# Optimization experiments

Measured on AMD Instinct MI355X. Metric: run time of the kernel, lower is better.

## Reference

```python
import jax, jax.numpy as jnp
import numpy as np

MODES1 = 16
MODES2 = 16
KX_SIGMA = 1.0
B, T, H, W, C = 4, 32, 128, 128, 1

KY_KERNEL = np.array([[0.01, 0.02, 0.04, 0.02, 0.01],
                      [0.02, 0.06, 0.09, 0.06, 0.02],
                      [0.04, 0.09, 0.16, 0.09, 0.04],
                      [0.02, 0.06, 0.09, 0.06, 0.02],
                      [0.01, 0.02, 0.04, 0.02, 0.01]], dtype=np.float32)


def _spectral_mix(x, w1, w2):
    # x: (B,T,H,W,C); w1,w2: complex (C,C,m1,m2). FFT-mode-truncated mixing.
    b, t, h, w, c = x.shape
    xc = jnp.transpose(x, (0, 1, 4, 2, 3))            # (B,T,C,H,W)
    x_ft = jnp.fft.rfft2(xc)                          # (B,T,C,H,W//2+1)
    wr = w // 2 + 1
    out_ft = jnp.zeros((b, t, c, h, wr), dtype=x_ft.dtype)
    top = jnp.einsum('btixy,ioxy->btoxy', x_ft[:, :, :, :MODES1, :MODES2], w1)
    bot = jnp.einsum('btixy,ioxy->btoxy', x_ft[:, :, :, h - MODES1:, :MODES2], w2)
    out_ft = out_ft.at[:, :, :, :MODES1, :MODES2].set(top)
    out_ft = out_ft.at[:, :, :, h - MODES1:, :MODES2].set(bot)
    out = jnp.fft.irfft2(out_ft, s=(h, w))            # (B,T,C,H,W)
    return jnp.transpose(out, (0, 1, 3, 4, 2))


def _restricted_spectral(x, scalar):
    # diagonal (identity * scalar) spectral weights == scale truncated modes
    b, t, h, w, c = x.shape
    xc = jnp.transpose(x, (0, 1, 4, 2, 3))
    x_ft = jnp.fft.rfft2(xc)
    wr = w // 2 + 1
    out_ft = jnp.zeros((b, t, c, h, wr), dtype=x_ft.dtype)
    out_ft = out_ft.at[:, :, :, :MODES1, :MODES2].set(x_ft[:, :, :, :MODES1, :MODES2] * scalar)
    out_ft = out_ft.at[:, :, :, h - MODES1:, :MODES2].set(x_ft[:, :, :, h - MODES1:, :MODES2] * scalar)
    out = jnp.fft.irfft2(out_ft, s=(h, w))
    return jnp.transpose(out, (0, 1, 3, 4, 2))


def _circular_conv(value, kernel):
    # value: (B,T,H,W,1), kernel: (kh,kw); circular-pad cross-correlation
    b, t, h, w, _ = value.shape
    kh, kw = kernel.shape
    x = value.reshape(b * t, 1, h, w)
    xp = jnp.pad(x, ((0, 0), (0, 0), (kh // 2, kh - kh // 2 - 1), (kw // 2, kw - kw // 2 - 1)), mode='wrap')
    out = jax.lax.conv_general_dilated(xp, kernel[None, None], (1, 1), 'VALID',
                                       dimension_numbers=('NCHW', 'OIHW', 'NCHW'))
    return out.reshape(b, t, h, w, 1)


def setup_inputs() -> dict:
    key = jax.random.key(0)
    ks = jax.random.split(key, 10)
    z = jax.random.normal(ks[0], (B, T, 2 * H, W, C), dtype=jnp.float32)
    scale = 1.0 / (C * C)  # torch: scale * torch.rand(cfloat) -> uniform real & imag
    u = lambda k: scale * jax.random.uniform(k, (C, C, MODES1, MODES2), dtype=jnp.float32)
    return {
        'z': z,
        'qw1r': u(ks[1]), 'qw1i': u(ks[2]), 'qw2r': u(ks[3]), 'qw2i': u(ks[4]),
        'kw1r': u(ks[5]), 'kw1i': u(ks[6]), 'kw2r': u(ks[7]), 'kw2i': u(ks[8]),
        'icl_scalar': jnp.float32(0.1),
        'ky_kernel': jnp.asarray(KY_KERNEL),
    }


def reference(z, qw1r, qw1i, qw2r, qw2i, kw1r, kw1i, kw2r, kw2i, icl_scalar, ky_kernel):
    b, t, full_h, w, c = z.shape
    h = full_h // 2
    x, y = z[:, :, :h], z[:, :, h:]
    query = _spectral_mix(x, qw1r + 1j * qw1i, qw2r + 1j * qw2i)
    keyt = _spectral_mix(x, kw1r + 1j * kw1i, kw2r + 1j * kw2i)
    value = _restricted_spectral(y, icl_scalar)
    # laplacian kernel attention scores
    q_ = query.reshape(b, t, -1)
    k_ = keyt.reshape(b, t, -1)
    diff = q_[:, :, None, :] - k_[:, None, :, :]        # (B,T,T,H*W*C)
    l2 = jnp.sqrt(jnp.sum(diff * diff, axis=-1) + 1e-8)
    kx = jnp.exp(-l2 / KX_SIGMA)                         # (B,T,T)
    # mask: M @ kx zeros out last query row
    mask = jnp.concatenate([jnp.ones((t - 1,), jnp.float32), jnp.zeros((1,), jnp.float32)])
    kx = kx * mask[None, :, None]
    vc = _circular_conv(value, ky_kernel)                # (B,T,H,W,1)
    attn_y = jnp.einsum('bthwc,btq->bqhwc', vc, kx)      # (B,T,H,W,1)
    output = jnp.concatenate([jnp.zeros_like(x), attn_y], axis=2)
    return output, kx
```

## Files before the change

### kernel.cpp

```cpp
#include <hip/hip_runtime.h>
#include <math.h>

#define FVC_OFF   0
#define PHIQ_OFF  131072
#define PHIK_OFF  262144
#define OUT_KX_OFF 4194304

#define TWOPI_128 0.049087385212340517f
#define OUT_SCALE 6.103515625e-05f

__global__ __launch_bounds__(256) void dft_rows_kernel(
    const float* __restrict__ z, float* __restrict__ Gout)
{
    __shared__ float2 tw[128];
    __shared__ float rows[16 * 132];
    __shared__ float2 tile[16 * 17];

    const int tid = threadIdx.x;
    const int img = blockIdx.x >> 3;
    const int c0  = blockIdx.x & 7;
    const int bt  = img & 127;
    const int isY = img >> 7;

    if (tid < 128) {
        float s, c;
        sincosf((float)tid * TWOPI_128, &s, &c);
        tw[tid] = make_float2(c, s);
    }
    const float* xim = z + (size_t)bt * 32768 + (size_t)isY * 16384 + (size_t)c0 * 2048;
    {
        int q0 = tid, q1 = tid + 256;
        float4 a = *(const float4*)(xim + (q0 >> 5) * 128 + (q0 & 31) * 4);
        float4 b = *(const float4*)(xim + (q1 >> 5) * 128 + (q1 & 31) * 4);
        *(float4*)(rows + (q0 >> 5) * 132 + (q0 & 31) * 4) = a;
        *(float4*)(rows + (q1 >> 5) * 132 + (q1 & 31) * 4) = b;
    }
    __syncthreads();

    const int v  = tid & 15;
    const int hl = tid >> 4;
    const float2 stp = tw[(4 * v) & 127];
    float cc = 1.f, ss = 0.f;
    float sr0 = 0.f, si0 = 0.f, sr1 = 0.f, si1 = 0.f;
    float sr2 = 0.f, si2 = 0.f, sr3 = 0.f, si3 = 0.f;
    const float4* rp = (const float4*)(rows + hl * 132);
    #pragma unroll 8
    for (int m = 0; m < 32; ++m) {
        float4 x4 = rp[m];
        sr0 = fmaf(x4.x, cc, sr0); si0 = fmaf(x4.x, ss, si0);
        sr1 = fmaf(x4.y, cc, sr1); si1 = fmaf(x4.y, ss, si1);
        sr2 = fmaf(x4.z, cc, sr2); si2 = fmaf(x4.z, ss, si2);
        sr3 = fmaf(x4.w, cc, sr3); si3 = fmaf(x4.w, ss, si3);
        float t0 = fmaf(cc, stp.x, -(ss * stp.y));
        float t1 = fmaf(cc, stp.y,  (ss * stp.x));
        cc = t0; ss = t1;
    }
    float2 w1 = tw[v];
    float2 w2 = tw[(2 * v) & 127];
    float2 w3 = tw[(3 * v) & 127];
    float gr = sr0 + sr1 * w1.x - si1 * w1.y + sr2 * w2.x - si2 * w2.y + sr3 * w3.x - si3 * w3.y;
    float gi = -(si0 + sr1 * w1.y + si1 * w1.x + sr2 * w2.y + si2 * w2.x + sr3 * w3.y + si3 * w3.x);

    tile[v * 17 + hl] = make_float2(gr, gi);
    __syncthreads();
    const int vw = tid >> 4, hw = tid & 15;
    float2 val = tile[vw * 17 + hw];
    *(float2*)(Gout + (size_t)img * 4096 + vw * 256 + (c0 * 16 + hw) * 2) = val;
}

__global__ __launch_bounds__(128) void modes_kernel(
    const float* __restrict__ Gglob,
    const float* __restrict__ qw1r, const float* __restrict__ qw1i,
    const float* __restrict__ qw2r, const float* __restrict__ qw2i,
    const float* __restrict__ kw1r, const float* __restrict__ kw1i,
    const float* __restrict__ kw2r, const float* __restrict__ kw2i,
    const float* __restrict__ icl,  const float* __restrict__ ker,
    float* __restrict__ ws)
{
    __shared__ float2 tw[128];
    __shared__ float Gbuf[4 * 260];
    __shared__ float f0r[64], f0i[64];

    const int tid = threadIdx.x;
    const int img = blockIdx.x >> 2;
    const int vg  = blockIdx.x & 3;
    const int bt  = img & 127;
    const int isY = img >> 7;

    {
        float s, c;
        sincosf((float)tid * TWOPI_128, &s, &c);
        tw[tid] = make_float2(c, s);
    }
    const float4* gsrc = (const float4*)(Gglob + (size_t)img * 4096 + (size_t)vg * 1024);
    {
        float4 a = gsrc[tid];
        float4 b = gsrc[tid + 128];
        *(float4*)(Gbuf + (tid >> 6) * 260 + (tid & 63) * 4) = a;
        *(float4*)(Gbuf + ((tid >> 6) + 2) * 260 + (tid & 63) * 4) = b;
    }
    __syncthreads();

    const int uu = tid & 31;
    const int vl = tid >> 5;
    const int v  = vg * 4 + vl;
    const int u  = (uu < 16) ? uu : uu + 96;

    const float2 stp = tw[(4 * u) & 127];
    float cc = 1.f, ss = 0.f;
    float sr[4] = {0.f, 0.f, 0.f, 0.f}, si[4] = {0.f, 0.f, 0.f, 0.f};
    const float4* gp = (const float4*)(Gbuf + vl * 260);
    #pragma unroll 8
    for (int m = 0; m < 32; ++m) {
        float4 ga = gp[2 * m];
        float4 gb = gp[2 * m + 1];
        sr[0] = fmaf(ga.x, cc, fmaf(ga.y,  ss, sr[0]));
        si[0] = fmaf(ga.y, cc, fmaf(-ga.x, ss, si[0]));
        sr[1] = fmaf(ga.z, cc, fmaf(ga.w,  ss, sr[1]));
        si[1] = fmaf(ga.w, cc, fmaf(-ga.z, ss, si[1]));
        sr[2] = fmaf(gb.x, cc, fmaf(gb.y,  ss, sr[2]));
        si[2] = fmaf(gb.y, cc, fmaf(-gb.x, ss, si[2]));
        sr[3] = fmaf(gb.z, cc, fmaf(gb.w,  ss, sr[3]));
        si[3] = fmaf(gb.w, cc, fmaf(-gb.z, ss, si[3]));
        float t0 = fmaf(cc, stp.x, -(ss * stp.y));
        float t1 = fmaf(cc, stp.y,  (ss * stp.x));
        cc = t0; ss = t1;
    }
    float mr = sr[0], mi_ = si[0];
    #pragma unroll
    for (int j = 1; j < 4; ++j) {
        float2 wj = tw[(u * j) & 127];
        mr  += sr[j] * wj.x + si[j] * wj.y;
        mi_ += si[j] * wj.x - sr[j] * wj.y;
    }

    const int wi = (uu & 15) * 16 + v;

    if (!isY) {
        float a, bi_;
        if (uu < 16) { a = qw1r[wi]; bi_ = qw1i[wi]; }
        else         { a = qw2r[wi]; bi_ = qw2i[wi]; }
        float fqr = mr * a - mi_ * bi_;
        float fqi = mr * bi_ + mi_ * a;
        if (uu < 16) { a = kw1r[wi]; bi_ = kw1i[wi]; }
        else         { a = kw2r[wi]; bi_ = kw2i[wi]; }
        float fkr = mr * a - mi_ * bi_;
        float fki = mr * bi_ + mi_ * a;

        float* PQ = ws + PHIQ_OFF + (size_t)bt * 1024;
        float* PK = ws + PHIK_OFF + (size_t)bt * 1024;
        const float c2 = 0.011048543456039806f;
        if (v >= 1) {
            int o = ((v - 1) * 32 + uu) * 2;
            PQ[o] = c2 * fqr; PQ[o + 1] = c2 * fqi;
            PK[o] = c2 * fkr; PK[o + 1] = c2 * fki;
        } else {
            f0r[uu]      = fqr; f0i[uu]      = fqi;
            f0r[32 + uu] = fkr; f0i[32 + uu] = fki;
        }
        __syncthreads();
        if (vg == 0) {
            const float c1n = 0.0078125f;
            if (tid == 0) {
                PQ[960] = c1n * f0r[0];
                PK[960] = c1n * f0r[32];
            } else if (tid <= 15) {
                int uf = tid;
                float hr = 0.5f * (f0r[uf] + f0r[32 - uf]);
                float hi = 0.5f * (f0i[uf] - f0i[32 - uf]);
                int o = 961 + (uf - 1) * 2;
                PQ[o] = c2 * hr; PQ[o + 1] = c2 * hi;
                hr = 0.5f * (f0r[32 + uf] + f0r[32 + (32 - uf)]);
                hi = 0.5f * (f0i[32 + uf] - f0i[32 + (32 - uf)]);
                PK[o] = c2 * hr; PK[o + 1] = c2 * hi;
            } else if (tid == 16) {
                PQ[991] = c2 * 0.5f * f0r[16]; PQ[992] = -c2 * 0.5f * f0i[16];
                PK[991] = c2 * 0.5f * f0r[48]; PK[992] = -c2 * 0.5f * f0i[48];
            } else if (tid < 48) {
                PQ[993 + (tid - 17)] = 0.f;
                PK[993 + (tid - 17)] = 0.f;
            }
        }
    } else {
        float s = icl[0];
        float khr = 0.f, khi = 0.f;
        #pragma unroll
        for (int a2 = 0; a2 < 5; ++a2) {
            #pragma unroll
            for (int c3 = 0; c3 < 5; ++c3) {
                float kv = ker[a2 * 5 + c3];
                float2 e = tw[(u * (a2 - 2) + v * (c3 - 2)) & 127];
                khr = fmaf(kv, e.x, khr);
                khi = fmaf(kv, e.y, khi);
            }
        }
        const int slot = uu * 16 + v;
        float* FV = ws + FVC_OFF + (size_t)bt * 1024;
        FV[slot * 2]     = s * (mr * khr - mi_ * khi);
        FV[slot * 2 + 1] = s * (mr * khi + mi_ * khr);
    }
}

__global__ __launch_bounds__(256) void dist_mix_inv_kernel(
    const float* __restrict__ ws, float* __restrict__ out)
{
    __shared__ float2 tw[128];
    __shared__ float kxs[32];
    __shared__ float fmP[32 * 36];
    __shared__ float Az[32 * 36];

    const int tid     = threadIdx.x;
    const int b       = blockIdx.x >> 7;
    const int rest    = blockIdx.x & 127;
    const int q       = rest >> 2;
    const int quarter = rest & 3;
    const size_t obase = (size_t)(b * 32 + q) * 32768;

    if (tid < 128) {
        float s, c;
        sincosf((float)tid * TWOPI_128, &s, &c);
        tw[tid] = make_float2(c, s);
    }

    {
        const float4 z4 = make_float4(0.f, 0.f, 0.f, 0.f);
        #pragma unroll
        for (int k = 0; k < 4; ++k) {
            int idx = k * 256 + tid;
            *(float4*)(out + obase + (size_t)quarter * 4096 + (size_t)idx * 4) = z4;
        }
    }

    {
        const int t = tid >> 3, seg = tid & 7;
        const float4* qp = (const float4*)(ws + PHIQ_OFF + (size_t)(b * 32 + t) * 1024) + seg * 32;
        const float4* kp = (const float4*)(ws + PHIK_OFF + (size_t)(b * 32 + q) * 1024) + seg * 32;
        float acc = 0.f;
        #pragma unroll 8
        for (int d = 0; d < 32; ++d) {
            float4 qv = qp[d], kv = kp[d];
            float d0 = qv.x - kv.x, d1 = qv.y - kv.y;
            float d2 = qv.z - kv.z, d3 = qv.w - kv.w;
            acc = fmaf(d0, d0, acc); acc = fmaf(d1, d1, acc);
            acc = fmaf(d2, d2, acc); acc = fmaf(d3, d3, acc);
        }
        acc += __shfl_xor(acc, 1);
        acc += __shfl_xor(acc, 2);
        acc += __shfl_xor(acc, 4);
        if (seg == 0) {
            float l2  = sqrtf(acc + 1e-8f);
            float kxv = (t == 31) ? 0.f : expf(-l2);
            kxs[t] = kxv;
            if (quarter == 0)
                out[OUT_KX_OFF + (b * 32 + t) * 32 + q] = kxv;
        }
    }
    __syncthreads();

    {
        float4 acc = make_float4(0.f, 0.f, 0.f, 0.f);
        const float4* FV = (const float4*)(ws + FVC_OFF) + (size_t)b * 32 * 256;
        for (int i = 0; i < 31; ++i) {
            float kv = kxs[i];
            float4 f = FV[(size_t)i * 256 + tid];
            acc.x = fmaf(kv, f.x, acc.x);
            acc.y = fmaf(kv, f.y, acc.y);
            acc.z = fmaf(kv, f.z, acc.z);
            acc.w = fmaf(kv, f.w, acc.w);
        }
        int s0 = tid * 2;
        *(float4*)(fmP + (s0 >> 4) * 36 + (s0 & 15) * 2) = acc;
    }
    __syncthreads();

    {
        const int hl = tid >> 3;
        const int v0 = (tid & 7) * 2;
        const int h  = quarter * 32 + hl;
        const float2 stp = tw[h];
        float cA = 1.f, sA = 0.f;
        const float2 ib = tw[(112 * h) & 127];
        float cB = ib.x, sB = ib.y;
        float ar0 = 0.f, ai0 = 0.f, ar1 = 0.f, ai1 = 0.f;
        #pragma unroll 4
        for (int j = 0; j < 16; ++j) {
            float4 fa = *(const float4*)(fmP + j * 36 + v0 * 2);
            ar0 = fmaf(fa.x, cA, fmaf(-fa.y, sA, ar0));
            ai0 = fmaf(fa.x, sA, fmaf( fa.y, cA, ai0));
            ar1 = fmaf(fa.z, cA, fmaf(-fa.w, sA, ar1));
            ai1 = fmaf(fa.z, sA, fmaf( fa.w, cA, ai1));
            float4 fb = *(const float4*)(fmP + (j + 16) * 36 + v0 * 2);
            ar0 = fmaf(fb.x, cB, fmaf(-fb.y, sB, ar0));
            ai0 = fmaf(fb.x, sB, fmaf( fb.y, cB, ai0));
            ar1 = fmaf(fb.z, cB, fmaf(-fb.w, sB, ar1));
            ai1 = fmaf(fb.z, sB, fmaf( fb.w, cB, ai1));
            float t0 = fmaf(cA, stp.x, -(sA * stp.y));
            float t1 = fmaf(cA, stp.y,  (sA * stp.x));
            cA = t0; sA = t1;
            t0 = fmaf(cB, stp.x, -(sB * stp.y));
            t1 = fmaf(cB, stp.y,  (sB * stp.x));
            cB = t0; sB = t1;
        }
        *(float4*)(Az + hl * 36 + v0 * 2) = make_float4(ar0, ai0, ar1, ai1);
    }

    const int wv   = tid >> 6;
    const int lane = tid & 63;
    float cw[16], sw[16];
    #pragma unroll
    for (int v = 1; v < 16; ++v) {
        float2 t = tw[(v * lane) & 127];
        cw[v] = t.x; sw[v] = t.y;
    }
    __syncthreads();

    for (int lr = 0; lr < 8; ++lr) {
        int l = wv * 8 + lr;
        const float4* az = (const float4*)(Az + l * 36);
        float4 f0 = az[0];
        float base = f0.x;
        float accO = f0.z * cw[1] - f0.w * sw[1];
        float accE = 0.f;
        #pragma unroll
        for (int t2 = 1; t2 < 8; ++t2) {
            float4 f = az[t2];
            accE = fmaf(f.x, cw[2 * t2],     fmaf(-f.y, sw[2 * t2],     accE));
            accO = fmaf(f.z, cw[2 * t2 + 1], fmaf(-f.w, sw[2 * t2 + 1], accO));
        }
        float pA = base + 2.f * (accE + accO);
        float pB = base + 2.f * (accE - accO);
        int r = quarter * 32 + l;
        out[obase + (size_t)(128 + r) * 128 + lane]      = pA * OUT_SCALE;
        out[obase + (size_t)(128 + r) * 128 + lane + 64] = pB * OUT_SCALE;
    }
}

extern "C" void kernel_launch(void* const* d_in, const int* in_sizes, int n_in,
                              void* d_out, int out_size, void* d_ws, size_t ws_size,
                              hipStream_t stream)
{
    (void)in_sizes; (void)n_in; (void)out_size; (void)ws_size;
    const float* z    = (const float*)d_in[0];
    const float* qw1r = (const float*)d_in[1];
    const float* qw1i = (const float*)d_in[2];
    const float* qw2r = (const float*)d_in[3];
    const float* qw2i = (const float*)d_in[4];
    const float* kw1r = (const float*)d_in[5];
    const float* kw1i = (const float*)d_in[6];
    const float* kw2r = (const float*)d_in[7];
    const float* kw2i = (const float*)d_in[8];
    const float* icl  = (const float*)d_in[9];
    const float* ker  = (const float*)d_in[10];
    float* ws  = (float*)d_ws;
    float* out = (float*)d_out;

    hipLaunchKernelGGL(dft_rows_kernel, dim3(2048), dim3(256), 0, stream, z, out);
    hipLaunchKernelGGL(modes_kernel, dim3(1024), dim3(128), 0, stream,
                       out, qw1r, qw1i, qw2r, qw2i, kw1r, kw1i, kw2r, kw2i,
                       icl, ker, ws);
    hipLaunchKernelGGL(dist_mix_inv_kernel, dim3(512), dim3(256), 0, stream, ws, out);
}
```

Measured before the change: 117.1 us.

## Fuse row DFT and mode-mixing kernels into one per-image kernel

Merges the row-DFT kernel and the modes kernel into a single kernel with one 512-thread block per image. The intermediate spectrum stays in shared memory instead of a global round trip, and global loads of the next 32-row chunk are issued while the current chunk is transformed. The zeroing of the output's upper half moves into this kernel and out of the final kernel, and scattered scalar stores become float2 stores. In exchange the launch has only 256 blocks, down from 2048 and 1024, which lowers parallelism and occupancy.

```diff
diff --git a/kernel.cpp b/kernel.cpp
--- a/kernel.cpp
+++ b/kernel.cpp
@@ -9,107 +9,97 @@
 #define TWOPI_128 0.049087385212340517f
 #define OUT_SCALE 6.103515625e-05f
 
-__global__ __launch_bounds__(256) void dft_rows_kernel(
-    const float* __restrict__ z, float* __restrict__ Gout)
-{
-    __shared__ float2 tw[128];
-    __shared__ float rows[16 * 132];
-    __shared__ float2 tile[16 * 17];
-
-    const int tid = threadIdx.x;
-    const int img = blockIdx.x >> 3;
-    const int c0  = blockIdx.x & 7;
-    const int bt  = img & 127;
-    const int isY = img >> 7;
-
-    if (tid < 128) {
-        float s, c;
-        sincosf((float)tid * TWOPI_128, &s, &c);
-        tw[tid] = make_float2(c, s);
-    }
-    const float* xim = z + (size_t)bt * 32768 + (size_t)isY * 16384 + (size_t)c0 * 2048;
-    {
-        int q0 = tid, q1 = tid + 256;
-        float4 a = *(const float4*)(xim + (q0 >> 5) * 128 + (q0 & 31) * 4);
-        float4 b = *(const float4*)(xim + (q1 >> 5) * 128 + (q1 & 31) * 4);
-        *(float4*)(rows + (q0 >> 5) * 132 + (q0 & 31) * 4) = a;
-        *(float4*)(rows + (q1 >> 5) * 132 + (q1 & 31) * 4) = b;
-    }
-    __syncthreads();
-
-    const int v  = tid & 15;
-    const int hl = tid >> 4;
-    const float2 stp = tw[(4 * v) & 127];
-    float cc = 1.f, ss = 0.f;
-    float sr0 = 0.f, si0 = 0.f, sr1 = 0.f, si1 = 0.f;
-    float sr2 = 0.f, si2 = 0.f, sr3 = 0.f, si3 = 0.f;
-    const float4* rp = (const float4*)(rows + hl * 132);
-    #pragma unroll 8
-    for (int m = 0; m < 32; ++m) {
-        float4 x4 = rp[m];
-        sr0 = fmaf(x4.x, cc, sr0); si0 = fmaf(x4.x, ss, si0);
-        sr1 = fmaf(x4.y, cc, sr1); si1 = fmaf(x4.y, ss, si1);
-        sr2 = fmaf(x4.z, cc, sr2); si2 = fmaf(x4.z, ss, si2);
-        sr3 = fmaf(x4.w, cc, sr3); si3 = fmaf(x4.w, ss, si3);
-        float t0 = fmaf(cc, stp.x, -(ss * stp.y));
-        float t1 = fmaf(cc, stp.y,  (ss * stp.x));
-        cc = t0; ss = t1;
-    }
-    float2 w1 = tw[v];
-    float2 w2 = tw[(2 * v) & 127];
-    float2 w3 = tw[(3 * v) & 127];
-    float gr = sr0 + sr1 * w1.x - si1 * w1.y + sr2 * w2.x - si2 * w2.y + sr3 * w3.x - si3 * w3.y;
-    float gi = -(si0 + sr1 * w1.y + si1 * w1.x + sr2 * w2.y + si2 * w2.x + sr3 * w3.y + si3 * w3.x);
-
-    tile[v * 17 + hl] = make_float2(gr, gi);
-    __syncthreads();
-    const int vw = tid >> 4, hw = tid & 15;
-    float2 val = tile[vw * 17 + hw];
-    *(float2*)(Gout + (size_t)img * 4096 + vw * 256 + (c0 * 16 + hw) * 2) = val;
-}
-
-__global__ __launch_bounds__(128) void modes_kernel(
-    const float* __restrict__ Gglob,
+__global__ __launch_bounds__(512) void dft_modes_kernel(
+    const float* __restrict__ z,
     const float* __restrict__ qw1r, const float* __restrict__ qw1i,
     const float* __restrict__ qw2r, const float* __restrict__ qw2i,
     const float* __restrict__ kw1r, const float* __restrict__ kw1i,
     const float* __restrict__ kw2r, const float* __restrict__ kw2i,
     const float* __restrict__ icl,  const float* __restrict__ ker,
-    float* __restrict__ ws)
+    float* __restrict__ ws, float* __restrict__ out)
 {
     __shared__ float2 tw[128];
-    __shared__ float Gbuf[4 * 260];
+    __shared__ float rows[32 * 132];
+    __shared__ float Gs[16 * 260];
     __shared__ float f0r[64], f0i[64];
 
     const int tid = threadIdx.x;
-    const int img = blockIdx.x >> 2;
-    const int vg  = blockIdx.x & 3;
+    const int img = blockIdx.x;
     const int bt  = img & 127;
     const int isY = img >> 7;
 
     {
+        const float4 z4 = make_float4(0.f, 0.f, 0.f, 0.f);
+        float* zb = out + (size_t)bt * 32768 + (size_t)isY * 8192;
+        #pragma unroll
+        for (int k = 0; k < 4; ++k)
+            *(float4*)(zb + (size_t)(tid + k * 512) * 4) = z4;
+    }
+
+    if (tid < 128) {
         float s, c;
         sincosf((float)tid * TWOPI_128, &s, &c);
         tw[tid] = make_float2(c, s);
     }
-    const float4* gsrc = (const float4*)(Gglob + (size_t)img * 4096 + (size_t)vg * 1024);
-    {
-        float4 a = gsrc[tid];
-        float4 b = gsrc[tid + 128];
-        *(float4*)(Gbuf + (tid >> 6) * 260 + (tid & 63) * 4) = a;
-        *(float4*)(Gbuf + ((tid >> 6) + 2) * 260 + (tid & 63) * 4) = b;
+
+    const float* xim = z + (size_t)bt * 32768 + (size_t)isY * 16384;
+    const int half = tid >> 8;
+    const int t8   = tid & 255;
+    const int v1   = t8 & 15;
+    const int hl   = t8 >> 4;
+
+    float4 a0 = *(const float4*)(xim + (size_t)tid * 4);
+    float4 a1 = *(const float4*)(xim + (size_t)(tid + 512) * 4);
+
+    for (int p = 0; p < 4; ++p) {
+        __syncthreads();
+        {
+            const int q0 = tid, q1 = tid + 512;
+            *(float4*)(rows + (q0 >> 5) * 132 + (q0 & 31) * 4) = a0;
+            *(float4*)(rows + (q1 >> 5) * 132 + (q1 & 31) * 4) = a1;
+        }
+        if (p < 3) {
+            const float* nx = xim + (size_t)(p + 1) * 4096;
+            a0 = *(const float4*)(nx + (size_t)tid * 4);
+            a1 = *(const float4*)(nx + (size_t)(tid + 512) * 4);
+        }
+        __syncthreads();
+
+        const float2 stp = tw[(4 * v1) & 127];
+        float cc = 1.f, ss = 0.f;
+        float sr0 = 0.f, si0 = 0.f, sr1 = 0.f, si1 = 0.f;
+        float sr2 = 0.f, si2 = 0.f, sr3 = 0.f, si3 = 0.f;
+        const float4* rp = (const float4*)(rows + (half * 16 + hl) * 132);
+        #pragma unroll 8
+        for (int m = 0; m < 32; ++m) {
+            float4 x4 = rp[m];
+            sr0 = fmaf(x4.x, cc, sr0); si0 = fmaf(x4.x, ss, si0);
+            sr1 = fmaf(x4.y, cc, sr1); si1 = fmaf(x4.y, ss, si1);
+            sr2 = fmaf(x4.z, cc, sr2); si2 = fmaf(x4.z, ss, si2);
+            sr3 = fmaf(x4.w, cc, sr3); si3 = fmaf(x4.w, ss, si3);
+            float t0 = fmaf(cc, stp.x, -(ss * stp.y));
+            float t1 = fmaf(cc, stp.y,  (ss * stp.x));
+            cc = t0; ss = t1;
+        }
+        float2 w1 = tw[v1];
+        float2 w2 = tw[(2 * v1) & 127];
+        float2 w3 = tw[(3 * v1) & 127];
+        float gr = sr0 + sr1 * w1.x - si1 * w1.y + sr2 * w2.x - si2 * w2.y + sr3 * w3.x - si3 * w3.y;
+        float gi = -(si0 + sr1 * w1.y + si1 * w1.x + sr2 * w2.y + si2 * w2.x + sr3 * w3.y + si3 * w3.x);
+
+        const int h = (2 * p + half) * 16 + hl;
+        *(float2*)(Gs + v1 * 260 + h * 2) = make_float2(gr, gi);
     }
     __syncthreads();
 
     const int uu = tid & 31;
-    const int vl = tid >> 5;
-    const int v  = vg * 4 + vl;
+    const int v  = tid >> 5;
     const int u  = (uu < 16) ? uu : uu + 96;
 
-    const float2 stp = tw[(4 * u) & 127];
+    const float2 stp2 = tw[(4 * u) & 127];
     float cc = 1.f, ss = 0.f;
     float sr[4] = {0.f, 0.f, 0.f, 0.f}, si[4] = {0.f, 0.f, 0.f, 0.f};
-    const float4* gp = (const float4*)(Gbuf + vl * 260);
+    const float4* gp = (const float4*)(Gs + v * 260);
     #pragma unroll 8
     for (int m = 0; m < 32; ++m) {
         float4 ga = gp[2 * m];
@@ -122,8 +112,8 @@
         si[2] = fmaf(gb.y, cc, fmaf(-gb.x, ss, si[2]));
         sr[3] = fmaf(gb.z, cc, fmaf(gb.w,  ss, sr[3]));
         si[3] = fmaf(gb.w, cc, fmaf(-gb.z, ss, si[3]));
-        float t0 = fmaf(cc, stp.x, -(ss * stp.y));
-        float t1 = fmaf(cc, stp.y,  (ss * stp.x));
+        float t0 = fmaf(cc, stp2.x, -(ss * stp2.y));
+        float t1 = fmaf(cc, stp2.y,  (ss * stp2.x));
         cc = t0; ss = t1;
     }
     float mr = sr[0], mi_ = si[0];
@@ -152,34 +142,32 @@
         const float c2 = 0.011048543456039806f;
         if (v >= 1) {
             int o = ((v - 1) * 32 + uu) * 2;
-            PQ[o] = c2 * fqr; PQ[o + 1] = c2 * fqi;
-            PK[o] = c2 * fkr; PK[o + 1] = c2 * fki;
+            *(float2*)(PQ + o) = make_float2(c2 * fqr, c2 * fqi);
+            *(float2*)(PK + o) = make_float2(c2 * fkr, c2 * fki);
         } else {
             f0r[uu]      = fqr; f0i[uu]      = fqi;
             f0r[32 + uu] = fkr; f0i[32 + uu] = fki;
         }
         __syncthreads();
-        if (vg == 0) {
-            const float c1n = 0.0078125f;
-            if (tid == 0) {
-                PQ[960] = c1n * f0r[0];
-                PK[960] = c1n * f0r[32];
-            } else if (tid <= 15) {
-                int uf = tid;
-                float hr = 0.5f * (f0r[uf] + f0r[32 - uf]);
-                float hi = 0.5f * (f0i[uf] - f0i[32 - uf]);
-                int o = 961 + (uf - 1) * 2;
-                PQ[o] = c2 * hr; PQ[o + 1] = c2 * hi;
-                hr = 0.5f * (f0r[32 + uf] + f0r[32 + (32 - uf)]);
-                hi = 0.5f * (f0i[32 + uf] - f0i[32 + (32 - uf)]);
-                PK[o] = c2 * hr; PK[o + 1] = c2 * hi;
-            } else if (tid == 16) {
-                PQ[991] = c2 * 0.5f * f0r[16]; PQ[992] = -c2 * 0.5f * f0i[16];
-                PK[991] = c2 * 0.5f * f0r[48]; PK[992] = -c2 * 0.5f * f0i[48];
-            } else if (tid < 48) {
-                PQ[993 + (tid - 17)] = 0.f;
-                PK[993 + (tid - 17)] = 0.f;
-            }
+        const float c1n = 0.0078125f;
+        if (tid == 0) {
+            PQ[960] = c1n * f0r[0];
+            PK[960] = c1n * f0r[32];
+        } else if (tid <= 15) {
+            int uf = tid;
+            float hr = 0.5f * (f0r[uf] + f0r[32 - uf]);
+            float hi = 0.5f * (f0i[uf] - f0i[32 - uf]);
+            int o = 961 + (uf - 1) * 2;
+            PQ[o] = c2 * hr; PQ[o + 1] = c2 * hi;
+            hr = 0.5f * (f0r[32 + uf] + f0r[32 + (32 - uf)]);
+            hi = 0.5f * (f0i[32 + uf] - f0i[32 + (32 - uf)]);
+            PK[o] = c2 * hr; PK[o + 1] = c2 * hi;
+        } else if (tid == 16) {
+            PQ[991] = c2 * 0.5f * f0r[16]; PQ[992] = -c2 * 0.5f * f0i[16];
+            PK[991] = c2 * 0.5f * f0r[48]; PK[992] = -c2 * 0.5f * f0i[48];
+        } else if (tid < 48) {
+            PQ[993 + (tid - 17)] = 0.f;
+            PK[993 + (tid - 17)] = 0.f;
         }
     } else {
         float s = icl[0];
@@ -196,8 +184,8 @@
         }
         const int slot = uu * 16 + v;
         float* FV = ws + FVC_OFF + (size_t)bt * 1024;
-        FV[slot * 2]     = s * (mr * khr - mi_ * khi);
-        FV[slot * 2 + 1] = s * (mr * khi + mi_ * khr);
+        *(float2*)(FV + slot * 2) =
+            make_float2(s * (mr * khr - mi_ * khi), s * (mr * khi + mi_ * khr));
     }
 }
 
@@ -220,15 +208,6 @@
         float s, c;
         sincosf((float)tid * TWOPI_128, &s, &c);
         tw[tid] = make_float2(c, s);
-    }
-
-    {
-        const float4 z4 = make_float4(0.f, 0.f, 0.f, 0.f);
-        #pragma unroll
-        for (int k = 0; k < 4; ++k) {
-            int idx = k * 256 + tid;
-            *(float4*)(out + obase + (size_t)quarter * 4096 + (size_t)idx * 4) = z4;
-        }
     }
 
     {
@@ -354,9 +333,8 @@
     float* ws  = (float*)d_ws;
     float* out = (float*)d_out;
 
-    hipLaunchKernelGGL(dft_rows_kernel, dim3(2048), dim3(256), 0, stream, z, out);
-    hipLaunchKernelGGL(modes_kernel, dim3(1024), dim3(128), 0, stream,
-                       out, qw1r, qw1i, qw2r, qw2i, kw1r, kw1i, kw2r, kw2i,
-                       icl, ker, ws);
+    hipLaunchKernelGGL(dft_modes_kernel, dim3(256), dim3(512), 0, stream,
+                       z, qw1r, qw1i, qw2r, qw2i, kw1r, kw1i, kw2r, kw2i,
+                       icl, ker, ws, out);
     hipLaunchKernelGGL(dist_mix_inv_kernel, dim3(512), dim3(256), 0, stream, ws, out);
 }
```

Result: no change. 117.7 us (+0.5%).
